# Kernel optimization log

Hardware: AMD Instinct MI355X
Metric: run time of the kernel (lower is better)

## Reference

```python
import jax, jax.numpy as jnp
import numpy as np

WS = 7        # window_size
SHIFT = 3     # shift_size
NH = 12       # num_heads
HD = 32       # head_dim
C = 384       # dim
HH = 56       # height
WW = 56       # width
EPS = 1e-5


def _rel_pos_index():
    coords = np.stack(np.meshgrid(np.arange(WS), np.arange(WS), indexing='ij')).reshape(2, -1)
    rel = (coords[:, :, None] - coords[:, None, :]).transpose(1, 2, 0)
    rel[:, :, 0] += WS - 1
    rel[:, :, 1] += WS - 1
    rel[:, :, 0] *= 2 * WS - 1
    return rel.sum(-1)  # (49, 49) int


def _attn_mask():
    # shift mask, computed statically (shift_size > 0 path)
    img = np.zeros((HH, WW))
    slices = (slice(0, -WS), slice(-WS, -SHIFT), slice(-SHIFT, None))
    cnt = 0
    for hs in slices:
        for ws in slices:
            img[hs, ws] = cnt
            cnt += 1
    mw = img.reshape(HH // WS, WS, WW // WS, WS).transpose(0, 2, 1, 3).reshape(-1, WS * WS)
    diff = mw[:, None, :] - mw[:, :, None]  # (nW, 49, 49)
    return np.where(diff != 0, -100.0, 0.0).astype(np.float32)


_REL_IDX = jnp.asarray(_rel_pos_index())
_MASK = jnp.asarray(_attn_mask())


def _layernorm(x, g, b):
    mu = jnp.mean(x, axis=-1, keepdims=True)
    var = jnp.mean(jnp.square(x - mu), axis=-1, keepdims=True)
    return (x - mu) * jax.lax.rsqrt(var + EPS) * g + b


def setup_inputs() -> dict:
    key = jax.random.key(0)
    ks = jax.random.split(key, 10)
    s = 0.02
    return {
        'hidden_states': jax.random.normal(ks[0], (32, HH * WW, C), jnp.float32),
        'ln1_g': jnp.ones((C,), jnp.float32),
        'ln1_b': jnp.zeros((C,), jnp.float32),
        'qkv_w': jax.random.normal(ks[1], (3 * C, C), jnp.float32) * s,
        'qkv_b': jnp.zeros((3 * C,), jnp.float32),
        'out_w': jax.random.normal(ks[2], (C, C), jnp.float32) * s,
        'out_b': jnp.zeros((C,), jnp.float32),
        'rel_bias_table': jax.random.normal(ks[3], ((2 * WS - 1) ** 2, NH), jnp.float32) * s,
        'ln2_g': jnp.ones((C,), jnp.float32),
        'ln2_b': jnp.zeros((C,), jnp.float32),
        'fc1_w': jax.random.normal(ks[4], (4 * C, C), jnp.float32) * s,
        'fc1_b': jnp.zeros((4 * C,), jnp.float32),
        'fc2_w': jax.random.normal(ks[5], (C, 4 * C), jnp.float32) * s,
        'fc2_b': jnp.zeros((C,), jnp.float32),
        'height': HH,
        'width': WW,
    }


def reference(hidden_states, ln1_g, ln1_b, qkv_w, qkv_b, out_w, out_b,
              rel_bias_table, ln2_g, ln2_b, fc1_w, fc1_b, fc2_w, fc2_b,
              height, width):
    B = hidden_states.shape[0]
    nWh, nWw = HH // WS, WW // WS
    nW = nWh * nWw
    L = WS * WS

    shortcut = hidden_states
    x = _layernorm(hidden_states, ln1_g, ln1_b).reshape(B, HH, WW, C)
    x = jnp.roll(x, (-SHIFT, -SHIFT), axis=(1, 2))
    # window partition -> (B*nW, 49, C)
    xw = x.reshape(B, nWh, WS, nWw, WS, C).transpose(0, 1, 3, 2, 4, 5).reshape(B * nW, L, C)

    qkv = xw @ qkv_w.T + qkv_b
    q, k, v = jnp.split(qkv, 3, axis=-1)
    q = q.reshape(-1, L, NH, HD).transpose(0, 2, 1, 3)  # (N, h, 49, d)
    k = k.reshape(-1, L, NH, HD).transpose(0, 2, 1, 3)
    v = v.reshape(-1, L, NH, HD).transpose(0, 2, 1, 3)

    scale = HD ** -0.5
    attn = jnp.einsum('nhqd,nhkd->nhqk', q, k) * scale
    bias = rel_bias_table[_REL_IDX.reshape(-1)].reshape(L, L, NH).transpose(2, 0, 1)  # (h, 49, 49)
    attn = attn + bias[None]
    attn = attn.reshape(B, nW, NH, L, L) + _MASK[None, :, None]
    attn = jax.nn.softmax(attn, axis=-1).reshape(B * nW, NH, L, L)

    out = jnp.einsum('nhqk,nhkd->nhqd', attn, v).transpose(0, 2, 1, 3).reshape(B * nW, L, C)
    out = out @ out_w.T + out_b

    # window reverse + un-shift
    out = out.reshape(B, nWh, nWw, WS, WS, C).transpose(0, 1, 3, 2, 4, 5).reshape(B, HH, WW, C)
    out = jnp.roll(out, (SHIFT, SHIFT), axis=(1, 2)).reshape(B, HH * WW, C)

    x = shortcut + out  # drop_path is identity (rate 0 / eval)
    h2 = _layernorm(x, ln2_g, ln2_b)
    mlp = jax.nn.gelu(h2 @ fc1_w.T + fc1_b, approximate=False) @ fc2_w.T + fc2_b
    return x + mlp
```

## Files before the change

kernel.cpp:

```cpp
#include <hip/hip_runtime.h>
#include <cstdint>
#include <cstddef>

using u16 = unsigned short;
using u32 = unsigned int;

typedef __attribute__((ext_vector_type(8))) short bf16x8;
typedef __attribute__((ext_vector_type(4))) float f32x4;

__device__ __forceinline__ u16 f2bf(float f) {
  union { float f; u32 u; } v; v.f = f;
  u32 r = v.u + 0x7FFFu + ((v.u >> 16) & 1u);
  return (u16)(r >> 16);
}
__device__ __forceinline__ float bf2f(u16 h) {
  union { u32 u; float f; } v; v.u = ((u32)h) << 16;
  return v.f;
}

__device__ __forceinline__ void gl_lds16(const void* g, void* l) {
  __builtin_amdgcn_global_load_lds(
      (const __attribute__((address_space(1))) void*)g,
      (__attribute__((address_space(3))) void*)l, 16, 0, 0);
}

__global__ __launch_bounds__(256) void k_f2bf(const float* __restrict__ s,
                                              u16* __restrict__ d, int n) {
  int i = blockIdx.x * 256 + threadIdx.x;
  if (i < n) d[i] = f2bf(s[i]);
}

__global__ __launch_bounds__(256) void k_tbl(const float* __restrict__ relt,
                                             float* __restrict__ tbl) {
  int id = blockIdx.x * 256 + threadIdx.x;
  if (id >= 196608) return;
  int i = id & 63, j = (id >> 6) & 63;
  int wt = (id >> 12) & 3, h = id >> 14;
  float v;
  if (j >= 49) {
    v = -3e38f;
  } else {
    int ii = i < 49 ? i : 48;
    int r1 = ii / 7, c1 = ii % 7, r2 = j / 7, c2 = j % 7;
    v = relt[((r1 - r2 + 6) * 13 + (c1 - c2 + 6)) * 12 + h];
    int rr1 = (wt & 2) ? (r1 < 4 ? 1 : 2) : 0;
    int rr2 = (wt & 2) ? (r2 < 4 ? 1 : 2) : 0;
    int cc1 = (wt & 1) ? (c1 < 4 ? 1 : 2) : 0;
    int cc2 = (wt & 1) ? (c2 < 4 ? 1 : 2) : 0;
    if (rr1 != rr2 || cc1 != cc2) v -= 100.f;
  }
  tbl[id] = v;
}

template <int GATHER>
__global__ __launch_bounds__(256) void k_ln(const float* __restrict__ x,
                                            const float* __restrict__ g,
                                            const float* __restrict__ b,
                                            u16* __restrict__ out) {
  int wave = threadIdx.x >> 6, lane = threadIdx.x & 63;
  int idx = blockIdx.x * 4 + wave;
  int src;
  if (GATHER) {
    int n = idx / 49, l = idx % 49;
    int bb = n >> 6, wi = n & 63;
    int wh = wi >> 3, ww = wi & 7;
    int r = l / 7, c = l % 7;
    int sr = wh * 7 + r + 3; if (sr >= 56) sr -= 56;
    int sc = ww * 7 + c + 3; if (sc >= 56) sc -= 56;
    src = bb * 3136 + sr * 56 + sc;
  } else {
    src = idx;
  }
  const float* xi = x + (size_t)src * 384;
  float2 v[3];
  float s = 0.f, sq = 0.f;
#pragma unroll
  for (int p = 0; p < 3; ++p) {
    v[p] = *(const float2*)(xi + p * 128 + lane * 2);
    s += v[p].x + v[p].y;
    sq += v[p].x * v[p].x + v[p].y * v[p].y;
  }
#pragma unroll
  for (int o = 32; o; o >>= 1) {
    s += __shfl_xor(s, o);
    sq += __shfl_xor(sq, o);
  }
  float mu = s * (1.f / 384.f);
  float var = sq * (1.f / 384.f) - mu * mu;
  float rstd = rsqrtf(var + 1e-5f);
  u16* oo = out + (size_t)idx * 384;
#pragma unroll
  for (int p = 0; p < 3; ++p) {
    int e = p * 128 + lane * 2;
    u16 o0 = f2bf((v[p].x - mu) * rstd * g[e] + b[e]);
    u16 o1 = f2bf((v[p].y - mu) * rstd * g[e + 1] + b[e + 1]);
    u32 pk = (u32)o0 | ((u32)o1 << 16);
    *(u32*)(oo + e) = pk;
  }
}

enum { EPI_QKV = 0, EPI_PROJ = 1, EPI_GELU = 2, EPI_FC2 = 3 };

template <int EPI>
__global__ __launch_bounds__(256) void k_gemm(
    const u16* __restrict__ A, const u16* __restrict__ Bw,
    const float* __restrict__ bias, u16* __restrict__ obf,
    float* __restrict__ of32, const float* __restrict__ addsrc,
    int K, int lda, int ldb, int ldc, int NT) {
  __shared__ u16 As[2][128 * 64];
  __shared__ u16 Bs[2][128 * 64];
  const int nwg = gridDim.x;
  const int q = nwg >> 3, r = nwg & 7;
  const int xcd = blockIdx.x & 7, rank = blockIdx.x >> 3;
  const int swz = (xcd < r ? xcd * (q + 1) : r * (q + 1) + (xcd - r) * q) + rank;
  const int m0 = (swz / NT) * 128, n0 = (swz % NT) * 128;

  const int tid = threadIdx.x;
  const int w = tid >> 6, lane = tid & 63;
  const int wr = w >> 1, wc = w & 1;

  const int srow = 8 * w + (lane >> 3);
  const int scol = 8 * ((lane & 7) ^ (lane >> 3));
  const int dstw = w * 512;
  const size_t abase = (size_t)(m0 + srow) * lda + scol;
  const size_t bbase = (size_t)(n0 + srow) * ldb + scol;

  f32x4 acc[4][4] = {};
  const int lrow = lane & 15;
  const int g8 = (lane >> 4) * 8;
  const int rxor = (lrow & 7) << 3;

  const int NTK = K >> 6;
#pragma unroll
  for (int i = 0; i < 4; ++i)
    gl_lds16(A + abase + (size_t)(32 * i) * lda, &As[0][i * 2048 + dstw]);
#pragma unroll
  for (int i = 0; i < 4; ++i)
    gl_lds16(Bw + bbase + (size_t)(32 * i) * ldb, &Bs[0][i * 2048 + dstw]);

  for (int t = 0; t < NTK; ++t) {
    const int cur = t & 1;
    if (t + 1 < NTK) {
      const int k1 = (t + 1) << 6;
#pragma unroll
      for (int i = 0; i < 4; ++i)
        gl_lds16(A + abase + (size_t)(32 * i) * lda + k1,
                 &As[cur ^ 1][i * 2048 + dstw]);
#pragma unroll
      for (int i = 0; i < 4; ++i)
        gl_lds16(Bw + bbase + (size_t)(32 * i) * ldb + k1,
                 &Bs[cur ^ 1][i * 2048 + dstw]);
      asm volatile("s_waitcnt vmcnt(8)" ::: "memory");
    } else {
      asm volatile("s_waitcnt vmcnt(0)" ::: "memory");
    }
    __builtin_amdgcn_s_barrier();
    asm volatile("" ::: "memory");
    __builtin_amdgcn_s_setprio(1);
#pragma unroll
    for (int kk = 0; kk < 64; kk += 32) {
      bf16x8 af[4], bf[4];
#pragma unroll
      for (int mi = 0; mi < 4; ++mi) {
        int row = wr * 64 + mi * 16 + lrow;
        af[mi] = *(const bf16x8*)(&As[cur][row * 64 + ((kk + g8) ^ rxor)]);
      }
#pragma unroll
      for (int ni = 0; ni < 4; ++ni) {
        int row = wc * 64 + ni * 16 + lrow;
        bf[ni] = *(const bf16x8*)(&Bs[cur][row * 64 + ((kk + g8) ^ rxor)]);
      }
#pragma unroll
      for (int mi = 0; mi < 4; ++mi)
#pragma unroll
        for (int ni = 0; ni < 4; ++ni)
          acc[mi][ni] = __builtin_amdgcn_mfma_f32_16x16x32_bf16(
              af[mi], bf[ni], acc[mi][ni], 0, 0, 0);
    }
    __builtin_amdgcn_s_setprio(0);
    asm volatile("" ::: "memory");
    __builtin_amdgcn_s_barrier();
    asm volatile("" ::: "memory");
  }

  const int erow = (lane >> 4) * 4;
  const int ecol = lane & 15;
#pragma unroll
  for (int mi = 0; mi < 4; ++mi) {
#pragma unroll
    for (int ni = 0; ni < 4; ++ni) {
      int gcol = n0 + wc * 64 + ni * 16 + ecol;
      float bv = bias[gcol];
#pragma unroll
      for (int r4 = 0; r4 < 4; ++r4) {
        int grow = m0 + wr * 64 + mi * 16 + erow + r4;
        float v = acc[mi][ni][r4] + bv;
        if (EPI == EPI_QKV) {
          float vv = (gcol < 384) ? v * 0.17677669529663689f : v;
          obf[(size_t)grow * ldc + gcol] = f2bf(vv);
        } else if (EPI == EPI_GELU) {
          float gl = 0.5f * v * (1.f + erff(v * 0.70710678118f));
          obf[(size_t)grow * ldc + gcol] = f2bf(gl);
        } else if (EPI == EPI_PROJ) {
          int nwin = grow / 49, l = grow % 49;
          int bb = nwin >> 6, wi = nwin & 63;
          int wh = wi >> 3, ww = wi & 7;
          int rr = l / 7, cc = l % 7;
          int sr = wh * 7 + rr + 3; if (sr >= 56) sr -= 56;
          int sc = ww * 7 + cc + 3; if (sc >= 56) sc -= 56;
          size_t idx = ((size_t)(bb * 3136 + sr * 56 + sc)) * 384 + gcol;
          of32[idx] = addsrc[idx] + v;
        } else {
          size_t idx = (size_t)grow * 384 + gcol;
          of32[idx] = of32[idx] + v;
        }
      }
    }
  }
}

__global__ __launch_bounds__(64) void k_attn2(const u16* __restrict__ qkv,
                                              const float* __restrict__ tbl,
                                              u16* __restrict__ out) {
  __shared__ u16 P[64 * 64];
  const int bx = blockIdx.x;
  const int n = bx / 12, h = bx - n * 12;
  const int lane = threadIdx.x & 63;
  const int g = lane >> 4, c = lane & 15;
  const u16* base = qkv + (size_t)n * 56448 + h * 32;
  const int wi = n & 63;
  const int wt = (((wi >> 3) == 7) ? 2 : 0) | (((wi & 7) == 7) ? 1 : 0);
  const float* T = tbl + (size_t)((h << 2) | wt) * 4096;

  f32x4 st[4][4];
#pragma unroll
  for (int kj = 0; kj < 4; ++kj)
#pragma unroll
    for (int qi = 0; qi < 4; ++qi)
#pragma unroll
      for (int r = 0; r < 4; ++r)
        st[kj][qi][r] = T[(kj * 16 + g * 4 + r) * 64 + qi * 16 + c];

  bf16x8 qf[4], kf[4];
#pragma unroll
  for (int t = 0; t < 4; ++t) {
    int row = t * 16 + c; if (row > 48) row = 48;
    qf[t] = *(const bf16x8*)(base + (size_t)row * 1152 + g * 8);
    kf[t] = *(const bf16x8*)(base + (size_t)row * 1152 + 384 + g * 8);
  }

#pragma unroll
  for (int kj = 0; kj < 4; ++kj)
#pragma unroll
    for (int qi = 0; qi < 4; ++qi)
      st[kj][qi] = __builtin_amdgcn_mfma_f32_16x16x32_bf16(kf[kj], qf[qi],
                                                           st[kj][qi], 0, 0, 0);

#pragma unroll
  for (int qi = 0; qi < 4; ++qi) {
    float m = -3e38f;
#pragma unroll
    for (int kj = 0; kj < 4; ++kj)
#pragma unroll
      for (int r = 0; r < 4; ++r) m = fmaxf(m, st[kj][qi][r]);
    m = fmaxf(m, __shfl_xor(m, 16));
    m = fmaxf(m, __shfl_xor(m, 32));
    float sum = 0.f;
#pragma unroll
    for (int kj = 0; kj < 4; ++kj)
#pragma unroll
      for (int r = 0; r < 4; ++r) {
        float e = __expf(st[kj][qi][r] - m);
        st[kj][qi][r] = e;
        sum += e;
      }
    sum += __shfl_xor(sum, 16);
    sum += __shfl_xor(sum, 32);
    float inv = 1.f / sum;
    int i = qi * 16 + c;
#pragma unroll
    for (int kj = 0; kj < 4; ++kj)
#pragma unroll
      for (int hh = 0; hh < 2; ++hh) {
        u32 pk = (u32)f2bf(st[kj][qi][2 * hh] * inv) |
                 ((u32)f2bf(st[kj][qi][2 * hh + 1] * inv) << 16);
        int idx = (i * 64 + kj * 16 + g * 4 + 2 * hh) ^ ((i & 7) << 3);
        *(u32*)(P + idx) = pk;
      }
  }

  f32x4 o[4][2] = {};
#pragma unroll
  for (int k0 = 0; k0 < 2; ++k0) {
    bf16x8 pa[4], vb[2];
#pragma unroll
    for (int qi = 0; qi < 4; ++qi) {
      int qq = qi * 16 + c;
      pa[qi] = *(const bf16x8*)(P + ((qq * 64 + k0 * 32 + g * 8) ^ ((qq & 7) << 3)));
    }
#pragma unroll
    for (int ni = 0; ni < 2; ++ni) {
      union { bf16x8 v; u16 a[8]; } vu;
#pragma unroll
      for (int e = 0; e < 8; ++e) {
        int j = k0 * 32 + g * 8 + e;
        int jr = j > 48 ? 48 : j;
        vu.a[e] = base[(size_t)jr * 1152 + 768 + ni * 16 + c];
      }
      vb[ni] = vu.v;
#pragma unroll
      for (int qi = 0; qi < 4; ++qi)
        o[qi][ni] = __builtin_amdgcn_mfma_f32_16x16x32_bf16(pa[qi], vb[ni],
                                                            o[qi][ni], 0, 0, 0);
    }
  }

  u16* ob = out + (size_t)n * 18816 + h * 32;
#pragma unroll
  for (int qi = 0; qi < 4; ++qi)
#pragma unroll
    for (int r = 0; r < 4; ++r) {
      int qq = qi * 16 + g * 4 + r;
      if (qq < 49) {
#pragma unroll
        for (int ni = 0; ni < 2; ++ni)
          ob[(size_t)qq * 384 + ni * 16 + c] = f2bf(o[qi][ni][r]);
      }
    }
}

extern "C" void kernel_launch(void* const* d_in, const int* in_sizes, int n_in,
                              void* d_out, int out_size, void* d_ws,
                              size_t ws_size, hipStream_t stream) {
  const float* hidden = (const float*)d_in[0];
  const float* ln1g = (const float*)d_in[1];
  const float* ln1b = (const float*)d_in[2];
  const float* qkvw = (const float*)d_in[3];
  const float* qkvb = (const float*)d_in[4];
  const float* outw = (const float*)d_in[5];
  const float* outb = (const float*)d_in[6];
  const float* relt = (const float*)d_in[7];
  const float* ln2g = (const float*)d_in[8];
  const float* ln2b = (const float*)d_in[9];
  const float* fc1w = (const float*)d_in[10];
  const float* fc1b = (const float*)d_in[11];
  const float* fc2w = (const float*)d_in[12];
  const float* fc2b = (const float*)d_in[13];
  float* out = (float*)d_out;

  u16* wq = (u16*)d_ws;
  u16* wo = wq + 442368;
  u16* w1 = wo + 147456;
  u16* w2 = w1 + 589824;
  u16* xw = w2 + 589824;
  u16* qkv = xw + 38535168;
  u16* xn = qkv;
  u16* hbuf = xn + 38535168;
  float* tbl = (float*)wq;

  k_f2bf<<<(442368 + 255) / 256, 256, 0, stream>>>(qkvw, wq, 442368);
  k_f2bf<<<(147456 + 255) / 256, 256, 0, stream>>>(outw, wo, 147456);
  k_f2bf<<<(589824 + 255) / 256, 256, 0, stream>>>(fc1w, w1, 589824);
  k_f2bf<<<(589824 + 255) / 256, 256, 0, stream>>>(fc2w, w2, 589824);

  k_ln<1><<<25088, 256, 0, stream>>>(hidden, ln1g, ln1b, xw);

  k_gemm<EPI_QKV><<<784 * 9, 256, 0, stream>>>(
      xw, wq, qkvb, qkv, nullptr, nullptr, 384, 384, 384, 1152, 9);

  k_tbl<<<768, 256, 0, stream>>>(relt, tbl);

  k_attn2<<<24576, 64, 0, stream>>>(qkv, tbl, xw);

  k_gemm<EPI_PROJ><<<784 * 3, 256, 0, stream>>>(
      xw, wo, outb, nullptr, out, hidden, 384, 384, 384, 384, 3);

  k_ln<0><<<25088, 256, 0, stream>>>(out, ln2g, ln2b, xn);

  for (int ch = 0; ch < 2; ++ch) {
    const u16* xa = xn + (size_t)ch * 50176 * 384;
    float* oc = out + (size_t)ch * 50176 * 384;
    k_gemm<EPI_GELU><<<392 * 12, 256, 0, stream>>>(
        xa, w1, fc1b, hbuf, nullptr, nullptr, 384, 384, 384, 1536, 12);
    k_gemm<EPI_FC2><<<392 * 3, 256, 0, stream>>>(
        hbuf, w2, fc2b, nullptr, oc, nullptr, 1536, 1536, 1536, 384, 3);
  }
}
```

Before: 968.5 us.

## Enlarge GEMM tiles to 256xBN with 8-wave workgroups and padded QKV weights

Replaces the 128x128, 4-wave GEMM with a templated 256xBN kernel using 512 threads. It uses BN=256 for QKV and FC1 and BN=128 for proj and FC2. The QKV weight is zero-padded to 1280 rows so N tiles evenly, and an Nmax guard skips out-of-range columns in the epilogue. The K loop now issues next-tile loads, runs MFMAs from register-cached B fragments, and waits for the loads at the end of each iteration. The aim is more data reuse per LDS/global load and fewer workgroups. The cost is a much larger LDS footprint (up to 128KB), which limits occupancy and latency hiding.

Measured after the change: 1.144 ms. 18.1% more time.

```diff
diff --git a/kernel.cpp b/kernel.cpp
--- a/kernel.cpp
+++ b/kernel.cpp
@@ -25,9 +25,10 @@
 }
 
 __global__ __launch_bounds__(256) void k_f2bf(const float* __restrict__ s,
-                                              u16* __restrict__ d, int n) {
+                                              u16* __restrict__ d, int n,
+                                              int npad) {
   int i = blockIdx.x * 256 + threadIdx.x;
-  if (i < n) d[i] = f2bf(s[i]);
+  if (i < npad) d[i] = (i < n) ? f2bf(s[i]) : (u16)0;
 }
 
 __global__ __launch_bounds__(256) void k_tbl(const float* __restrict__ relt,
@@ -101,99 +102,110 @@
 
 enum { EPI_QKV = 0, EPI_PROJ = 1, EPI_GELU = 2, EPI_FC2 = 3 };
 
-template <int EPI>
-__global__ __launch_bounds__(256) void k_gemm(
+template <int EPI, int BN>
+__global__ __launch_bounds__(512, 2) void k_gemm2(
     const u16* __restrict__ A, const u16* __restrict__ Bw,
     const float* __restrict__ bias, u16* __restrict__ obf,
     float* __restrict__ of32, const float* __restrict__ addsrc,
-    int K, int lda, int ldb, int ldc, int NT) {
-  __shared__ u16 As[2][128 * 64];
-  __shared__ u16 Bs[2][128 * 64];
+    int K, int lda, int ldb, int ldc, int NT, int Nmax) {
+  __shared__ u16 As[2][256 * 64];
+  __shared__ u16 Bs[2][BN * 64];
   const int nwg = gridDim.x;
   const int q = nwg >> 3, r = nwg & 7;
   const int xcd = blockIdx.x & 7, rank = blockIdx.x >> 3;
   const int swz = (xcd < r ? xcd * (q + 1) : r * (q + 1) + (xcd - r) * q) + rank;
-  const int m0 = (swz / NT) * 128, n0 = (swz % NT) * 128;
+  const int m0 = (swz / NT) * 256, n0 = (swz % NT) * BN;
 
   const int tid = threadIdx.x;
-  const int w = tid >> 6, lane = tid & 63;
-  const int wr = w >> 1, wc = w & 1;
-
-  const int srow = 8 * w + (lane >> 3);
-  const int scol = 8 * ((lane & 7) ^ (lane >> 3));
-  const int dstw = w * 512;
+  const int wid = tid >> 6, lane = tid & 63;
+  constexpr int MR = (BN == 256) ? 8 : 4;
+  constexpr int WM = (BN == 256) ? 128 : 64;
+  const int wr = (BN == 256) ? (wid >> 2) : (wid >> 1);
+  const int wc = (BN == 256) ? (wid & 3) : (wid & 1);
+
+  const int srow = tid >> 3;
+  const int scol = 8 * ((tid & 7) ^ (srow & 7));
   const size_t abase = (size_t)(m0 + srow) * lda + scol;
   const size_t bbase = (size_t)(n0 + srow) * ldb + scol;
-
-  f32x4 acc[4][4] = {};
+  const int dbase = wid * 512;
+
+  f32x4 acc[MR][4] = {};
   const int lrow = lane & 15;
   const int g8 = (lane >> 4) * 8;
-  const int rxor = (lrow & 7) << 3;
+  const int rx = (lrow & 7) << 3;
 
   const int NTK = K >> 6;
+
 #pragma unroll
   for (int i = 0; i < 4; ++i)
-    gl_lds16(A + abase + (size_t)(32 * i) * lda, &As[0][i * 2048 + dstw]);
-#pragma unroll
-  for (int i = 0; i < 4; ++i)
-    gl_lds16(Bw + bbase + (size_t)(32 * i) * ldb, &Bs[0][i * 2048 + dstw]);
+    gl_lds16(A + abase + (size_t)(i * 64) * lda, &As[0][i * 4096 + dbase]);
+#pragma unroll
+  for (int i = 0; i < BN / 64; ++i)
+    gl_lds16(Bw + bbase + (size_t)(i * 64) * ldb, &Bs[0][i * 4096 + dbase]);
+  asm volatile("s_waitcnt vmcnt(0)" ::: "memory");
+  __builtin_amdgcn_s_barrier();
+  asm volatile("" ::: "memory");
 
   for (int t = 0; t < NTK; ++t) {
     const int cur = t & 1;
     if (t + 1 < NTK) {
-      const int k1 = (t + 1) << 6;
+      const size_t k1 = (size_t)(t + 1) << 6;
 #pragma unroll
       for (int i = 0; i < 4; ++i)
-        gl_lds16(A + abase + (size_t)(32 * i) * lda + k1,
-                 &As[cur ^ 1][i * 2048 + dstw]);
-#pragma unroll
-      for (int i = 0; i < 4; ++i)
-        gl_lds16(Bw + bbase + (size_t)(32 * i) * ldb + k1,
-                 &Bs[cur ^ 1][i * 2048 + dstw]);
-      asm volatile("s_waitcnt vmcnt(8)" ::: "memory");
-    } else {
-      asm volatile("s_waitcnt vmcnt(0)" ::: "memory");
-    }
+        gl_lds16(A + abase + (size_t)(i * 64) * lda + k1,
+                 &As[cur ^ 1][i * 4096 + dbase]);
+#pragma unroll
+      for (int i = 0; i < BN / 64; ++i)
+        gl_lds16(Bw + bbase + (size_t)(i * 64) * ldb + k1,
+                 &Bs[cur ^ 1][i * 4096 + dbase]);
+    }
+    bf16x8 bfr[4][2];
+#pragma unroll
+    for (int n = 0; n < 4; ++n)
+#pragma unroll
+      for (int kh = 0; kh < 2; ++kh) {
+        int row = wc * 64 + n * 16 + lrow;
+        bfr[n][kh] = *(const bf16x8*)(&Bs[cur][row * 64 + ((kh * 32 + g8) ^ rx)]);
+      }
+#pragma unroll
+    for (int mh = 0; mh < MR / 4; ++mh) {
+      bf16x8 afr[4][2];
+#pragma unroll
+      for (int mq = 0; mq < 4; ++mq)
+#pragma unroll
+        for (int kh = 0; kh < 2; ++kh) {
+          int row = wr * WM + mh * 64 + mq * 16 + lrow;
+          afr[mq][kh] =
+              *(const bf16x8*)(&As[cur][row * 64 + ((kh * 32 + g8) ^ rx)]);
+        }
+      __builtin_amdgcn_s_setprio(1);
+#pragma unroll
+      for (int mq = 0; mq < 4; ++mq)
+#pragma unroll
+        for (int n = 0; n < 4; ++n)
+#pragma unroll
+          for (int kh = 0; kh < 2; ++kh)
+            acc[mh * 4 + mq][n] = __builtin_amdgcn_mfma_f32_16x16x32_bf16(
+                afr[mq][kh], bfr[n][kh], acc[mh * 4 + mq][n], 0, 0, 0);
+      __builtin_amdgcn_s_setprio(0);
+    }
+    asm volatile("s_waitcnt vmcnt(0)" ::: "memory");
     __builtin_amdgcn_s_barrier();
     asm volatile("" ::: "memory");
-    __builtin_amdgcn_s_setprio(1);
-#pragma unroll
-    for (int kk = 0; kk < 64; kk += 32) {
-      bf16x8 af[4], bf[4];
-#pragma unroll
-      for (int mi = 0; mi < 4; ++mi) {
-        int row = wr * 64 + mi * 16 + lrow;
-        af[mi] = *(const bf16x8*)(&As[cur][row * 64 + ((kk + g8) ^ rxor)]);
-      }
-#pragma unroll
-      for (int ni = 0; ni < 4; ++ni) {
-        int row = wc * 64 + ni * 16 + lrow;
-        bf[ni] = *(const bf16x8*)(&Bs[cur][row * 64 + ((kk + g8) ^ rxor)]);
-      }
-#pragma unroll
-      for (int mi = 0; mi < 4; ++mi)
-#pragma unroll
-        for (int ni = 0; ni < 4; ++ni)
-          acc[mi][ni] = __builtin_amdgcn_mfma_f32_16x16x32_bf16(
-              af[mi], bf[ni], acc[mi][ni], 0, 0, 0);
-    }
-    __builtin_amdgcn_s_setprio(0);
-    asm volatile("" ::: "memory");
-    __builtin_amdgcn_s_barrier();
-    asm volatile("" ::: "memory");
   }
 
   const int erow = (lane >> 4) * 4;
   const int ecol = lane & 15;
 #pragma unroll
-  for (int mi = 0; mi < 4; ++mi) {
+  for (int mi = 0; mi < MR; ++mi) {
 #pragma unroll
     for (int ni = 0; ni < 4; ++ni) {
       int gcol = n0 + wc * 64 + ni * 16 + ecol;
+      if (gcol >= Nmax) continue;
       float bv = bias[gcol];
 #pragma unroll
       for (int r4 = 0; r4 < 4; ++r4) {
-        int grow = m0 + wr * 64 + mi * 16 + erow + r4;
+        int grow = m0 + wr * WM + mi * 16 + erow + r4;
         float v = acc[mi][ni][r4] + bv;
         if (EPI == EPI_QKV) {
           float vv = (gcol < 384) ? v * 0.17677669529663689f : v;
@@ -349,7 +361,7 @@
   float* out = (float*)d_out;
 
   u16* wq = (u16*)d_ws;
-  u16* wo = wq + 442368;
+  u16* wo = wq + 491520;
   u16* w1 = wo + 147456;
   u16* w2 = w1 + 589824;
   u16* xw = w2 + 589824;
@@ -358,31 +370,31 @@
   u16* hbuf = xn + 38535168;
   float* tbl = (float*)wq;
 
-  k_f2bf<<<(442368 + 255) / 256, 256, 0, stream>>>(qkvw, wq, 442368);
-  k_f2bf<<<(147456 + 255) / 256, 256, 0, stream>>>(outw, wo, 147456);
-  k_f2bf<<<(589824 + 255) / 256, 256, 0, stream>>>(fc1w, w1, 589824);
-  k_f2bf<<<(589824 + 255) / 256, 256, 0, stream>>>(fc2w, w2, 589824);
+  k_f2bf<<<1920, 256, 0, stream>>>(qkvw, wq, 442368, 491520);
+  k_f2bf<<<576, 256, 0, stream>>>(outw, wo, 147456, 147456);
+  k_f2bf<<<2304, 256, 0, stream>>>(fc1w, w1, 589824, 589824);
+  k_f2bf<<<2304, 256, 0, stream>>>(fc2w, w2, 589824, 589824);
 
   k_ln<1><<<25088, 256, 0, stream>>>(hidden, ln1g, ln1b, xw);
 
-  k_gemm<EPI_QKV><<<784 * 9, 256, 0, stream>>>(
-      xw, wq, qkvb, qkv, nullptr, nullptr, 384, 384, 384, 1152, 9);
+  k_gemm2<EPI_QKV, 256><<<392 * 5, 512, 0, stream>>>(
+      xw, wq, qkvb, qkv, nullptr, nullptr, 384, 384, 384, 1152, 5, 1152);
 
   k_tbl<<<768, 256, 0, stream>>>(relt, tbl);
 
   k_attn2<<<24576, 64, 0, stream>>>(qkv, tbl, xw);
 
-  k_gemm<EPI_PROJ><<<784 * 3, 256, 0, stream>>>(
-      xw, wo, outb, nullptr, out, hidden, 384, 384, 384, 384, 3);
+  k_gemm2<EPI_PROJ, 128><<<392 * 3, 512, 0, stream>>>(
+      xw, wo, outb, nullptr, out, hidden, 384, 384, 384, 384, 3, 384);
 
   k_ln<0><<<25088, 256, 0, stream>>>(out, ln2g, ln2b, xn);
 
   for (int ch = 0; ch < 2; ++ch) {
     const u16* xa = xn + (size_t)ch * 50176 * 384;
     float* oc = out + (size_t)ch * 50176 * 384;
-    k_gemm<EPI_GELU><<<392 * 12, 256, 0, stream>>>(
-        xa, w1, fc1b, hbuf, nullptr, nullptr, 384, 384, 384, 1536, 12);
-    k_gemm<EPI_FC2><<<392 * 3, 256, 0, stream>>>(
-        hbuf, w2, fc2b, nullptr, oc, nullptr, 1536, 1536, 1536, 384, 3);
-  }
-}
+    k_gemm2<EPI_GELU, 256><<<196 * 6, 512, 0, stream>>>(
+        xa, w1, fc1b, hbuf, nullptr, nullptr, 384, 384, 384, 1536, 6, 1536);
+    k_gemm2<EPI_FC2, 128><<<196 * 3, 512, 0, stream>>>(
+        hbuf, w2, fc2b, nullptr, oc, nullptr, 1536, 1536, 1536, 384, 3, 384);
+  }
+}
```

## Switch GEMMs to 256x128 tiles with 8 waves, single-buffered LDS

Applied to the files above, without the earlier changes.

The GEMM kernel now uses 512-thread blocks with a 256x128 output tile instead of 128x128. B tiles are reused across twice as many rows. The LDS double buffering and explicit vmcnt prefetch pipeline are removed in favor of load, sync, compute, sync. Launch_bounds(512,2) is meant to let two blocks co-reside so their loads and compute overlap, but each block no longer overlaps its own global loads with its MFMA work.

Result: faster. 891.6 us (-7.9%).

```diff
diff --git a/kernel.cpp b/kernel.cpp
--- a/kernel.cpp
+++ b/kernel.cpp
@@ -102,60 +102,47 @@
 enum { EPI_QKV = 0, EPI_PROJ = 1, EPI_GELU = 2, EPI_FC2 = 3 };
 
 template <int EPI>
-__global__ __launch_bounds__(256) void k_gemm(
+__global__ __launch_bounds__(512, 2) void k_gemm3(
     const u16* __restrict__ A, const u16* __restrict__ Bw,
     const float* __restrict__ bias, u16* __restrict__ obf,
     float* __restrict__ of32, const float* __restrict__ addsrc,
     int K, int lda, int ldb, int ldc, int NT) {
-  __shared__ u16 As[2][128 * 64];
-  __shared__ u16 Bs[2][128 * 64];
+  __shared__ u16 As[256 * 64];
+  __shared__ u16 Bs[128 * 64];
   const int nwg = gridDim.x;
   const int q = nwg >> 3, r = nwg & 7;
   const int xcd = blockIdx.x & 7, rank = blockIdx.x >> 3;
   const int swz = (xcd < r ? xcd * (q + 1) : r * (q + 1) + (xcd - r) * q) + rank;
-  const int m0 = (swz / NT) * 128, n0 = (swz % NT) * 128;
+  const int m0 = (swz / NT) * 256, n0 = (swz % NT) * 128;
 
   const int tid = threadIdx.x;
-  const int w = tid >> 6, lane = tid & 63;
-  const int wr = w >> 1, wc = w & 1;
-
-  const int srow = 8 * w + (lane >> 3);
-  const int scol = 8 * ((lane & 7) ^ (lane >> 3));
-  const int dstw = w * 512;
+  const int wid = tid >> 6, lane = tid & 63;
+  const int wr = wid >> 1, wc = wid & 1;
+
+  const int srow = tid >> 3;
+  const int scol = 8 * ((tid & 7) ^ (srow & 7));
   const size_t abase = (size_t)(m0 + srow) * lda + scol;
   const size_t bbase = (size_t)(n0 + srow) * ldb + scol;
+  const int dbase = wid * 512;
 
   f32x4 acc[4][4] = {};
   const int lrow = lane & 15;
   const int g8 = (lane >> 4) * 8;
-  const int rxor = (lrow & 7) << 3;
+  const int rx = (lrow & 7) << 3;
 
   const int NTK = K >> 6;
-#pragma unroll
-  for (int i = 0; i < 4; ++i)
-    gl_lds16(A + abase + (size_t)(32 * i) * lda, &As[0][i * 2048 + dstw]);
-#pragma unroll
-  for (int i = 0; i < 4; ++i)
-    gl_lds16(Bw + bbase + (size_t)(32 * i) * ldb, &Bs[0][i * 2048 + dstw]);
 
   for (int t = 0; t < NTK; ++t) {
-    const int cur = t & 1;
-    if (t + 1 < NTK) {
-      const int k1 = (t + 1) << 6;
-#pragma unroll
-      for (int i = 0; i < 4; ++i)
-        gl_lds16(A + abase + (size_t)(32 * i) * lda + k1,
-                 &As[cur ^ 1][i * 2048 + dstw]);
-#pragma unroll
-      for (int i = 0; i < 4; ++i)
-        gl_lds16(Bw + bbase + (size_t)(32 * i) * ldb + k1,
-                 &Bs[cur ^ 1][i * 2048 + dstw]);
-      asm volatile("s_waitcnt vmcnt(8)" ::: "memory");
-    } else {
-      asm volatile("s_waitcnt vmcnt(0)" ::: "memory");
-    }
-    __builtin_amdgcn_s_barrier();
-    asm volatile("" ::: "memory");
+    const int k0 = t << 6;
+#pragma unroll
+    for (int i = 0; i < 4; ++i)
+      gl_lds16(A + abase + (size_t)(i * 64) * lda + k0,
+               As + i * 4096 + dbase);
+#pragma unroll
+    for (int i = 0; i < 2; ++i)
+      gl_lds16(Bw + bbase + (size_t)(i * 64) * ldb + k0,
+               Bs + i * 4096 + dbase);
+    __syncthreads();
     __builtin_amdgcn_s_setprio(1);
 #pragma unroll
     for (int kk = 0; kk < 64; kk += 32) {
@@ -163,12 +150,12 @@
 #pragma unroll
       for (int mi = 0; mi < 4; ++mi) {
         int row = wr * 64 + mi * 16 + lrow;
-        af[mi] = *(const bf16x8*)(&As[cur][row * 64 + ((kk + g8) ^ rxor)]);
+        af[mi] = *(const bf16x8*)(&As[row * 64 + ((kk + g8) ^ rx)]);
       }
 #pragma unroll
       for (int ni = 0; ni < 4; ++ni) {
         int row = wc * 64 + ni * 16 + lrow;
-        bf[ni] = *(const bf16x8*)(&Bs[cur][row * 64 + ((kk + g8) ^ rxor)]);
+        bf[ni] = *(const bf16x8*)(&Bs[row * 64 + ((kk + g8) ^ rx)]);
       }
 #pragma unroll
       for (int mi = 0; mi < 4; ++mi)
@@ -178,9 +165,7 @@
               af[mi], bf[ni], acc[mi][ni], 0, 0, 0);
     }
     __builtin_amdgcn_s_setprio(0);
-    asm volatile("" ::: "memory");
-    __builtin_amdgcn_s_barrier();
-    asm volatile("" ::: "memory");
+    __syncthreads();
   }
 
   const int erow = (lane >> 4) * 4;
@@ -358,21 +343,21 @@
   u16* hbuf = xn + 38535168;
   float* tbl = (float*)wq;
 
-  k_f2bf<<<(442368 + 255) / 256, 256, 0, stream>>>(qkvw, wq, 442368);
-  k_f2bf<<<(147456 + 255) / 256, 256, 0, stream>>>(outw, wo, 147456);
-  k_f2bf<<<(589824 + 255) / 256, 256, 0, stream>>>(fc1w, w1, 589824);
-  k_f2bf<<<(589824 + 255) / 256, 256, 0, stream>>>(fc2w, w2, 589824);
+  k_f2bf<<<1728, 256, 0, stream>>>(qkvw, wq, 442368);
+  k_f2bf<<<576, 256, 0, stream>>>(outw, wo, 147456);
+  k_f2bf<<<2304, 256, 0, stream>>>(fc1w, w1, 589824);
+  k_f2bf<<<2304, 256, 0, stream>>>(fc2w, w2, 589824);
 
   k_ln<1><<<25088, 256, 0, stream>>>(hidden, ln1g, ln1b, xw);
 
-  k_gemm<EPI_QKV><<<784 * 9, 256, 0, stream>>>(
+  k_gemm3<EPI_QKV><<<392 * 9, 512, 0, stream>>>(
       xw, wq, qkvb, qkv, nullptr, nullptr, 384, 384, 384, 1152, 9);
 
   k_tbl<<<768, 256, 0, stream>>>(relt, tbl);
 
   k_attn2<<<24576, 64, 0, stream>>>(qkv, tbl, xw);
 
-  k_gemm<EPI_PROJ><<<784 * 3, 256, 0, stream>>>(
+  k_gemm3<EPI_PROJ><<<392 * 3, 512, 0, stream>>>(
       xw, wo, outb, nullptr, out, hidden, 384, 384, 384, 384, 3);
 
   k_ln<0><<<25088, 256, 0, stream>>>(out, ln2g, ln2b, xn);
@@ -380,9 +365,9 @@
   for (int ch = 0; ch < 2; ++ch) {
     const u16* xa = xn + (size_t)ch * 50176 * 384;
     float* oc = out + (size_t)ch * 50176 * 384;
-    k_gemm<EPI_GELU><<<392 * 12, 256, 0, stream>>>(
+    k_gemm3<EPI_GELU><<<196 * 12, 512, 0, stream>>>(
         xa, w1, fc1b, hbuf, nullptr, nullptr, 384, 384, 384, 1536, 12);
-    k_gemm<EPI_FC2><<<392 * 3, 256, 0, stream>>>(
+    k_gemm3<EPI_FC2><<<196 * 3, 512, 0, stream>>>(
         hbuf, w2, fc2b, nullptr, oc, nullptr, 1536, 1536, 1536, 384, 3);
   }
 }
```
